# Kernel optimization log

Measured on AMD Instinct MI355X. Metric: run time of the kernel, lower is better.

Reference implementation:

```python
import jax, jax.numpy as jnp
import numpy as np
import math

B, S, D = 2, 2048, 768
H, KS, VS = 12, 64, 64
MAX_DIST, NUM_BASES, MIN_HALF_LIFE = 1000, 16, 3.0


def _exponential_basis_features():
    # positions -max_dist..max_dist, exponential basis as in RelativePositionalBias
    positions = np.arange(-MAX_DIST, MAX_DIST + 1)
    abs_pos = np.abs(positions).astype(np.float32)
    max_range = math.log2(MAX_DIST)
    half_lives = np.power(2.0, np.linspace(MIN_HALF_LIFE, max_range, NUM_BASES)).reshape(1, -1)
    feats = np.exp(-math.log(2.0) * abs_pos[:, None] / half_lives)  # [2*max_dist+1, num_bases]
    return jnp.asarray(feats, dtype=jnp.float32)


def setup_inputs() -> dict:
    key = jax.random.key(0)
    ks = jax.random.split(key, 6)
    x = jax.random.normal(ks[0], (B, S, D), dtype=jnp.float32)
    # torch nn.Linear weight convention: [out_features, in_features], applied as x @ W.T
    Wq = jax.random.normal(ks[1], (H * KS, D), dtype=jnp.float32) * 0.02
    Wk = jax.random.normal(ks[2], (H * KS, D), dtype=jnp.float32) * 0.02
    Wv = jax.random.normal(ks[3], (H * VS, D), dtype=jnp.float32) * 0.02
    # original zero-inits w_o; use small random for a non-degenerate correctness baseline
    Wo = jax.random.normal(ks[4], (D, H * VS), dtype=jnp.float32) * 0.02
    basis_weights = jax.random.normal(ks[5], (H, NUM_BASES), dtype=jnp.float32)
    basis_features = _exponential_basis_features()  # buffer (non-learned)
    return {"x": x, "Wq": Wq, "Wk": Wk, "Wv": Wv, "Wo": Wo,
            "basis_weights": basis_weights, "basis_features": basis_features}


def _relative_bias(basis_features, basis_weights, q_len, k_len):
    rel = jnp.arange(k_len)[None, :] - jnp.arange(q_len)[:, None]
    rel = jnp.clip(rel, -MAX_DIST, MAX_DIST) + MAX_DIST  # [q, k] indices
    basis = basis_features[rel]                          # [q, k, nb]
    return jnp.einsum('qkb,hb->hqk', basis, basis_weights)


def reference(x, Wq, Wk, Wv, Wo, basis_weights, basis_features):
    b, s, _ = x.shape
    q = (x @ Wq.T).reshape(b, s, H, KS)
    k = (x @ Wk.T).reshape(b, s, H, KS)
    v = (x @ Wv.T).reshape(b, s, H, VS)
    scale = math.sqrt(KS)
    scores = jnp.einsum('bqhc,bkhc->bhqk', q, k) / scale
    scores = scores + _relative_bias(basis_features, basis_weights, s, s)[None]
    attn = jax.nn.softmax(scores, axis=-1)  # dropout is identity in eval
    out = jnp.einsum('bhqk,bkhv->bqhv', attn, v).reshape(b, s, H * VS)
    out = out @ Wo.T
    return out, attn
```

## Files before the change

kernel.cpp:

```cpp
#include <hip/hip_runtime.h>

typedef _Float16 f16;
typedef __attribute__((ext_vector_type(8))) _Float16 f16x8;
typedef __attribute__((ext_vector_type(4))) float f32x4;
typedef __attribute__((ext_vector_type(16))) float f32x16;

#define B_ 2
#define S_ 2048
#define DMODEL 768
#define H_ 12
#define HS 64
#define NB_ 16
#define QKV_LD 2304

#define ZERO16 {0.f,0.f,0.f,0.f,0.f,0.f,0.f,0.f,0.f,0.f,0.f,0.f,0.f,0.f,0.f,0.f}

__device__ __forceinline__ void gload16(const f16* g, f16* lds) {
    __builtin_amdgcn_global_load_lds((const __attribute__((address_space(1))) void*)g,
                                     (__attribute__((address_space(3))) void*)lds, 16, 0, 0);
}

__global__ __launch_bounds__(256) void prep_kernel(const float* __restrict__ x,
                                                   const float* __restrict__ Wq,
                                                   const float* __restrict__ Wk,
                                                   const float* __restrict__ Wv,
                                                   const float* __restrict__ Wo,
                                                   const float* __restrict__ bw,
                                                   const float* __restrict__ bf,
                                                   f16* __restrict__ xb,
                                                   f16* __restrict__ wqkv16,
                                                   f16* __restrict__ wo16,
                                                   float* __restrict__ biasTab) {
    int bid = blockIdx.x;
    int t = threadIdx.x;
    if (bid < 5376) {
        const float* src;
        f16* dst;
        float scale = 1.0f;
        int i;
        if (bid < 3072) {
            i = bid * 256 + t; src = x; dst = xb;
        } else if (bid < 4800) {
            i = (bid - 3072) * 256 + t;
            dst = wqkv16;
            if (i < 147456)      { src = Wq; scale = 0.18033688011112f; }
            else if (i < 294912) { src = Wk - 147456 * 4; }
            else                 { src = Wv - 294912 * 4; }
        } else {
            i = (bid - 4800) * 256 + t; src = Wo; dst = wo16;
        }
        float4 v = reinterpret_cast<const float4*>(src)[i];
        union { f16 h[4]; unsigned long long u; } o;
        o.h[0] = (f16)(v.x * scale);
        o.h[1] = (f16)(v.y * scale);
        o.h[2] = (f16)(v.z * scale);
        o.h[3] = (f16)(v.w * scale);
        reinterpret_cast<unsigned long long*>(dst)[i] = o.u;
    } else {
        int idx = (bid - 5376) * 256 + t;
        if (idx >= H_ * 4095) return;
        int h = idx / 4095, d = idx % 4095;
        int rel = min(1000, max(-1000, d - 2047));
        int r = rel + 1000;
        float s = 0.f;
#pragma unroll
        for (int tt = 0; tt < NB_; ++tt) s += bf[r * NB_ + tt] * bw[h * NB_ + tt];
        biasTab[h * 4095 + d] = s * 1.44269504088896f;
    }
}

__global__ __launch_bounds__(256) void vtrans_kernel(const f16* __restrict__ qkv,
                                                     f16* __restrict__ vt) {
    __shared__ f16 tile[64][72];
    int blk = blockIdx.x;
    int tb = blk & 31;
    int bh = blk >> 5;
    int b = bh / H_;
    int tok0 = tb << 6;
    int t = threadIdx.x;
    const f16* src = qkv + (size_t)b * S_ * QKV_LD + 1536 + (bh - b * H_) * 64;
#pragma unroll
    for (int j = 0; j < 2; ++j) {
        int u = t + (j << 8);
        int r = u >> 3, c = (u & 7) << 3;
        *reinterpret_cast<f16x8*>(&tile[r][c]) =
            *reinterpret_cast<const f16x8*>(src + (size_t)(tok0 + r) * QKV_LD + c);
    }
    __syncthreads();
    f16* dst = vt + (size_t)bh * 64 * S_ + tok0;
#pragma unroll
    for (int j = 0; j < 2; ++j) {
        int u = t + (j << 8);
        int v = u >> 3, tc = (u & 7) << 3;
        union { f16 h8[8]; f16x8 v8; } o;
#pragma unroll
        for (int i = 0; i < 8; ++i) o.h8[i] = tile[tc + i][v];
        *reinterpret_cast<f16x8*>(&dst[(size_t)v * S_ + tc]) = o.v8;
    }
}

template <typename OutT>
__global__ __launch_bounds__(256) void gemm_nt(const f16* __restrict__ A,
                                               const f16* __restrict__ Bm,
                                               OutT* __restrict__ C,
                                               int M, int N, int K, float alpha) {
    __shared__ __align__(16) f16 As[128 * 32];
    __shared__ __align__(16) f16 Bs[128 * 32];
    const int tiles_n = N >> 7;
    int tm = blockIdx.x / tiles_n, tn = blockIdx.x % tiles_n;
    int m0 = tm << 7, n0 = tn << 7;
    int t = threadIdx.x;
    int w = t >> 6, l = t & 63;
    int wr = w >> 1, wc = w & 1;
    int fr = l & 15, hi = l >> 4;
    f32x4 acc[4][4] = {};

    for (int k0 = 0; k0 < K; k0 += 32) {
#pragma unroll
        for (int j = 0; j < 2; ++j) {
            int u = t + (j << 8);
            int row = u >> 2, ch = u & 3;
            int gcol = k0 + ((ch ^ (row & 3)) << 3);
            gload16(&A[(size_t)(m0 + row) * K + gcol], As + (w << 9) + (j << 11));
            gload16(&Bm[(size_t)(n0 + row) * K + gcol], Bs + (w << 9) + (j << 11));
        }
        __syncthreads();
        f16x8 af[4], bfv[4];
#pragma unroll
        for (int m = 0; m < 4; ++m) {
            int row = wr * 64 + m * 16 + fr;
            af[m] = *reinterpret_cast<const f16x8*>(&As[row * 32 + ((hi ^ (fr & 3)) << 3)]);
        }
#pragma unroll
        for (int n = 0; n < 4; ++n) {
            int row = wc * 64 + n * 16 + fr;
            bfv[n] = *reinterpret_cast<const f16x8*>(&Bs[row * 32 + ((hi ^ (fr & 3)) << 3)]);
        }
#pragma unroll
        for (int m = 0; m < 4; ++m)
#pragma unroll
            for (int n = 0; n < 4; ++n)
                acc[m][n] = __builtin_amdgcn_mfma_f32_16x16x32_f16(af[m], bfv[n], acc[m][n], 0, 0, 0);
        __syncthreads();
    }
    int cc = l & 15, cr = (l >> 4) << 2;
#pragma unroll
    for (int m = 0; m < 4; ++m)
#pragma unroll
        for (int n = 0; n < 4; ++n)
#pragma unroll
            for (int j = 0; j < 4; ++j) {
                int rg = m0 + wr * 64 + m * 16 + cr + j;
                int cg = n0 + wc * 64 + n * 16 + cc;
                C[(size_t)rg * N + cg] = (OutT)(acc[m][n][j] * alpha);
            }
}

__global__ __launch_bounds__(256, 4) void attn_kernel(const f16* __restrict__ qp,
                                                      const f16* __restrict__ kp,
                                                      const f16* __restrict__ vt,
                                                      const float* __restrict__ biasTab,
                                                      float* __restrict__ attn_out,
                                                      f16* __restrict__ ctx_out) {
    __shared__ __align__(16) union {
        f16 ks1[128 * 64];
        struct { f16 ks[64 * 64]; f16 vs[64 * 64]; } p2;
    } ar;
    __shared__ __align__(16) f16 psh[64][72];
    __shared__ float bias_l[2112];
    __shared__ float red_l[64][2];
    __shared__ float li_s[64];

    int orig = blockIdx.x;
    int blk = (orig & 7) * 96 + (orig >> 3);
    int qt = blk & 31;
    int bh = blk >> 5;
    int h = bh % H_;
    int b = bh / H_;
    int q0 = qt << 6;

    int t = threadIdx.x;
    int w = t >> 6, l = t & 63;
    int wq = w >> 1, wk = w & 1;
    int col = l & 31;
    int hi = l >> 5;
    int hi4 = hi << 2, hi8 = hi << 3;

    const size_t rowbase = (size_t)b * S_ * QKV_LD + (size_t)h * HS;
    const f16* vbase = vt + (size_t)bh * HS * S_;

    f16x8 qf[4];
    {
        const f16* qrow = qp + rowbase + (size_t)(q0 + wq * 32 + col) * QKV_LD + hi8;
#pragma unroll
        for (int ci = 0; ci < 4; ++ci) qf[ci] = *reinterpret_cast<const f16x8*>(qrow + ci * 16);
    }

    {
        const float* bt = biasTab + h * 4095 + (1984 - q0);
        for (int i = t; i < 2111; i += 256) bias_l[i] = bt[i];
    }

    float lsum[16];
#pragma unroll
    for (int r = 0; r < 16; ++r) lsum[r] = 0.f;

    for (int kb0 = 0; kb0 < S_; kb0 += 128) {
#pragma unroll
        for (int j = 0; j < 4; ++j) {
            int u = t + (j << 8);
            int row = u >> 3, ch = u & 7;
            gload16(kp + rowbase + (size_t)(kb0 + row) * QKV_LD + ((ch ^ (row & 7)) << 3),
                    ar.ks1 + (w << 9) + (j << 11));
        }
        __syncthreads();
#pragma unroll
        for (int half = 0; half < 2; ++half) {
            int krow = half * 64 + wk * 32 + col;
            f32x16 s = ZERO16;
#pragma unroll
            for (int ci = 0; ci < 4; ++ci) {
                f16x8 kf = *reinterpret_cast<const f16x8*>(
                    &ar.ks1[krow * 64 + (((ci * 2 + hi) ^ (col & 7)) << 3)]);
                s = __builtin_amdgcn_mfma_f32_32x32x16_f16(qf[ci], kf, s, 0, 0, 0);
            }
            int kcol = kb0 + krow;
            const float* bl = bias_l + (kcol + 63 - (wq * 32 + hi4));
#pragma unroll
            for (int r = 0; r < 16; ++r) {
                const int cr = (r & 3) + 8 * (r >> 2);
                lsum[r] += __builtin_amdgcn_exp2f(s[r] + bl[-cr]);
            }
        }
        __syncthreads();
    }

#pragma unroll
    for (int off = 1; off < 32; off <<= 1) {
#pragma unroll
        for (int r = 0; r < 16; ++r) lsum[r] += __shfl_xor(lsum[r], off);
    }
    if (col == 0) {
#pragma unroll
        for (int r = 0; r < 16; ++r)
            red_l[wq * 32 + (r & 3) + 8 * (r >> 2) + hi4][wk] = lsum[r];
    }
    __syncthreads();
    if (t < 64) li_s[t] = 1.0f / (red_l[t][0] + red_l[t][1]);
    __syncthreads();
    float lreg[16];
#pragma unroll
    for (int r = 0; r < 16; ++r) lreg[r] = li_s[wq * 32 + (r & 3) + 8 * (r >> 2) + hi4];

    f32x16 oacc = ZERO16;
    float* aout = attn_out + (((size_t)b * H_ + h) * S_ + q0) * S_;

    for (int kb0 = 0; kb0 < S_; kb0 += 64) {
#pragma unroll
        for (int j = 0; j < 2; ++j) {
            int u = t + (j << 8);
            int row = u >> 3, ch = u & 7;
            int sw = ((ch ^ (row & 7)) << 3);
            gload16(kp + rowbase + (size_t)(kb0 + row) * QKV_LD + sw,
                    ar.p2.ks + (w << 9) + (j << 11));
            gload16(vbase + (size_t)row * S_ + kb0 + sw,
                    ar.p2.vs + (w << 9) + (j << 11));
        }
        __syncthreads();
        int krow = wk * 32 + col;
        f32x16 s = ZERO16;
#pragma unroll
        for (int ci = 0; ci < 4; ++ci) {
            f16x8 kf = *reinterpret_cast<const f16x8*>(
                &ar.p2.ks[krow * 64 + (((ci * 2 + hi) ^ (col & 7)) << 3)]);
            s = __builtin_amdgcn_mfma_f32_32x32x16_f16(qf[ci], kf, s, 0, 0, 0);
        }
        int kcol = kb0 + krow;
        const float* bl = bias_l + (kcol + 63 - (wq * 32 + hi4));
#pragma unroll
        for (int r = 0; r < 16; ++r) {
            const int cr = (r & 3) + 8 * (r >> 2);
            int row = wq * 32 + cr + hi4;
            float p = __builtin_amdgcn_exp2f(s[r] + bl[-cr]) * lreg[r];
            __builtin_nontemporal_store(p, &aout[(size_t)row * S_ + kcol]);
            psh[row][wk * 32 + col] = (f16)p;
        }
        __syncthreads();
#pragma unroll
        for (int ci = 0; ci < 4; ++ci) {
            f16x8 pa = *reinterpret_cast<const f16x8*>(&psh[wq * 32 + col][ci * 16 + hi8]);
            f16x8 vf = *reinterpret_cast<const f16x8*>(
                &ar.p2.vs[krow * 64 + (((ci * 2 + hi) ^ (col & 7)) << 3)]);
            oacc = __builtin_amdgcn_mfma_f32_32x32x16_f16(pa, vf, oacc, 0, 0, 0);
        }
        __syncthreads();
    }

    {
        f16* cbase = ctx_out + ((size_t)b * S_ + q0) * DMODEL + h * HS + wk * 32 + col;
#pragma unroll
        for (int r = 0; r < 16; ++r) {
            int row = wq * 32 + (r & 3) + 8 * (r >> 2) + hi4;
            cbase[(size_t)row * DMODEL] = (f16)oacc[r];
        }
    }
}

extern "C" void kernel_launch(void* const* d_in, const int* in_sizes, int n_in,
                              void* d_out, int out_size, void* d_ws, size_t ws_size,
                              hipStream_t stream) {
    const float* x     = (const float*)d_in[0];
    const float* Wq    = (const float*)d_in[1];
    const float* Wk    = (const float*)d_in[2];
    const float* Wv    = (const float*)d_in[3];
    const float* Wo    = (const float*)d_in[4];
    const float* bw    = (const float*)d_in[5];
    const float* bfeat = (const float*)d_in[6];

    char* ws = (char*)d_ws;
    f16*   xb      = (f16*)(ws + 0);
    f16*   vt      = (f16*)(ws + 0);
    f16*   qkv     = (f16*)(ws + 6291456);
    f16*   ctx     = (f16*)(ws + 25165824);
    f16*   wqkv16  = (f16*)(ws + 31457280);
    f16*   wo16    = (f16*)(ws + 34996224);
    float* biasTab = (float*)(ws + 36175872);

    float* out0 = (float*)d_out;
    float* attn = out0 + (size_t)B_ * S_ * DMODEL;

    prep_kernel<<<5568, 256, 0, stream>>>(x, Wq, Wk, Wv, Wo, bw, bfeat,
                                          xb, wqkv16, wo16, biasTab);

    gemm_nt<f16><<<32 * 18, 256, 0, stream>>>(xb, wqkv16, qkv, 4096, QKV_LD, 768, 1.0f);

    vtrans_kernel<<<768, 256, 0, stream>>>(qkv, vt);

    attn_kernel<<<B_ * H_ * (S_ / 64), 256, 0, stream>>>(
        qkv + 0, qkv + 768, vt, biasTab, attn, ctx);

    gemm_nt<float><<<32 * 6, 256, 0, stream>>>(ctx, wo16, out0, 4096, DMODEL, 768, 1.0f);
}
```

Baseline: 177.7 us.

## Transpose QK MFMA so P stays in registers and attn stores vectorize

Swaps the MFMA operand order so each lane owns one query row and holds contiguous key columns. This lets the softmax row sum be a single per-lane scalar with one shuffle, turns the attention-probability stores into 16-byte vector stores, and feeds P to the PV MFMA through register shuffles instead of a shared-memory staging buffer. Each wave now computes partial outputs over all 64 value columns for its half of the keys, and the two halves are combined through shared memory at the end. The costs are extra accumulator registers and a final cross-wave reduction.

```diff
diff --git a/kernel.cpp b/kernel.cpp
--- a/kernel.cpp
+++ b/kernel.cpp
@@ -1,6 +1,8 @@
 #include <hip/hip_runtime.h>
 
 typedef _Float16 f16;
+typedef __attribute__((ext_vector_type(2))) __fp16 h16x2;
+typedef __attribute__((ext_vector_type(4))) _Float16 f16x4;
 typedef __attribute__((ext_vector_type(8))) _Float16 f16x8;
 typedef __attribute__((ext_vector_type(4))) float f32x4;
 typedef __attribute__((ext_vector_type(16))) float f32x16;
@@ -49,7 +51,7 @@
         } else {
             i = (bid - 4800) * 256 + t; src = Wo; dst = wo16;
         }
-        float4 v = reinterpret_cast<const float4*>(src)[i];
+        f32x4 v = reinterpret_cast<const f32x4*>(src)[i];
         union { f16 h[4]; unsigned long long u; } o;
         o.h[0] = (f16)(v.x * scale);
         o.h[1] = (f16)(v.y * scale);
@@ -165,11 +167,10 @@
     __shared__ __align__(16) union {
         f16 ks1[128 * 64];
         struct { f16 ks[64 * 64]; f16 vs[64 * 64]; } p2;
+        float red[4096];
     } ar;
-    __shared__ __align__(16) f16 psh[64][72];
     __shared__ float bias_l[2112];
     __shared__ float red_l[64][2];
-    __shared__ float li_s[64];
 
     int orig = blockIdx.x;
     int blk = (orig & 7) * 96 + (orig >> 3);
@@ -182,16 +183,16 @@
     int t = threadIdx.x;
     int w = t >> 6, l = t & 63;
     int wq = w >> 1, wk = w & 1;
-    int col = l & 31;
+    int ql = l & 31;
     int hi = l >> 5;
-    int hi4 = hi << 2, hi8 = hi << 3;
+    int hi8 = hi << 3;
 
     const size_t rowbase = (size_t)b * S_ * QKV_LD + (size_t)h * HS;
     const f16* vbase = vt + (size_t)bh * HS * S_;
 
     f16x8 qf[4];
     {
-        const f16* qrow = qp + rowbase + (size_t)(q0 + wq * 32 + col) * QKV_LD + hi8;
+        const f16* qrow = qp + rowbase + (size_t)(q0 + wq * 32 + ql) * QKV_LD + hi8;
 #pragma unroll
         for (int ci = 0; ci < 4; ++ci) qf[ci] = *reinterpret_cast<const f16x8*>(qrow + ci * 16);
     }
@@ -201,10 +202,7 @@
         for (int i = t; i < 2111; i += 256) bias_l[i] = bt[i];
     }
 
-    float lsum[16];
-#pragma unroll
-    for (int r = 0; r < 16; ++r) lsum[r] = 0.f;
-
+    float lsum = 0.f;
     for (int kb0 = 0; kb0 < S_; kb0 += 128) {
 #pragma unroll
         for (int j = 0; j < 4; ++j) {
@@ -214,46 +212,32 @@
                     ar.ks1 + (w << 9) + (j << 11));
         }
         __syncthreads();
+        const float* bl = bias_l + (kb0 + wk * 32 + 63 + (hi << 2) - wq * 32 - ql);
 #pragma unroll
         for (int half = 0; half < 2; ++half) {
-            int krow = half * 64 + wk * 32 + col;
+            int arow = half * 64 + wk * 32 + ql;
             f32x16 s = ZERO16;
 #pragma unroll
             for (int ci = 0; ci < 4; ++ci) {
                 f16x8 kf = *reinterpret_cast<const f16x8*>(
-                    &ar.ks1[krow * 64 + (((ci * 2 + hi) ^ (col & 7)) << 3)]);
-                s = __builtin_amdgcn_mfma_f32_32x32x16_f16(qf[ci], kf, s, 0, 0, 0);
+                    &ar.ks1[arow * 64 + (((ci * 2 + hi) ^ (arow & 7)) << 3)]);
+                s = __builtin_amdgcn_mfma_f32_32x32x16_f16(kf, qf[ci], s, 0, 0, 0);
             }
-            int kcol = kb0 + krow;
-            const float* bl = bias_l + (kcol + 63 - (wq * 32 + hi4));
-#pragma unroll
-            for (int r = 0; r < 16; ++r) {
-                const int cr = (r & 3) + 8 * (r >> 2);
-                lsum[r] += __builtin_amdgcn_exp2f(s[r] + bl[-cr]);
-            }
-        }
-        __syncthreads();
-    }
-
-#pragma unroll
-    for (int off = 1; off < 32; off <<= 1) {
-#pragma unroll
-        for (int r = 0; r < 16; ++r) lsum[r] += __shfl_xor(lsum[r], off);
-    }
-    if (col == 0) {
-#pragma unroll
-        for (int r = 0; r < 16; ++r)
-            red_l[wq * 32 + (r & 3) + 8 * (r >> 2) + hi4][wk] = lsum[r];
-    }
+            const float* blh = bl + half * 64;
+#pragma unroll
+            for (int r = 0; r < 16; ++r)
+                lsum += __builtin_amdgcn_exp2f(s[r] + blh[((r >> 2) << 3) + (r & 3)]);
+        }
+        __syncthreads();
+    }
+    lsum += __shfl_xor(lsum, 32);
+    if (hi == 0) red_l[wq * 32 + ql][wk] = lsum;
     __syncthreads();
-    if (t < 64) li_s[t] = 1.0f / (red_l[t][0] + red_l[t][1]);
-    __syncthreads();
-    float lreg[16];
-#pragma unroll
-    for (int r = 0; r < 16; ++r) lreg[r] = li_s[wq * 32 + (r & 3) + 8 * (r >> 2) + hi4];
-
-    f32x16 oacc = ZERO16;
-    float* aout = attn_out + (((size_t)b * H_ + h) * S_ + q0) * S_;
+    const float lreg = 1.0f / (red_l[wq * 32 + ql][0] + red_l[wq * 32 + ql][1]);
+
+    f32x16 oacc0 = ZERO16, oacc1 = ZERO16;
+    float* arow_out = attn_out + (((size_t)b * H_ + h) * S_ + q0) * S_
+                    + (size_t)(wq * 32 + ql) * S_;
 
     for (int kb0 = 0; kb0 < S_; kb0 += 64) {
 #pragma unroll
@@ -267,41 +251,81 @@
                     ar.p2.vs + (w << 9) + (j << 11));
         }
         __syncthreads();
-        int krow = wk * 32 + col;
+        int arow = wk * 32 + ql;
         f32x16 s = ZERO16;
 #pragma unroll
         for (int ci = 0; ci < 4; ++ci) {
             f16x8 kf = *reinterpret_cast<const f16x8*>(
-                &ar.p2.ks[krow * 64 + (((ci * 2 + hi) ^ (col & 7)) << 3)]);
-            s = __builtin_amdgcn_mfma_f32_32x32x16_f16(qf[ci], kf, s, 0, 0, 0);
-        }
-        int kcol = kb0 + krow;
-        const float* bl = bias_l + (kcol + 63 - (wq * 32 + hi4));
+                &ar.p2.ks[arow * 64 + (((ci * 2 + hi) ^ (arow & 7)) << 3)]);
+            s = __builtin_amdgcn_mfma_f32_32x32x16_f16(kf, qf[ci], s, 0, 0, 0);
+        }
+        const float* bl = bias_l + (kb0 + wk * 32 + 63 + (hi << 2) - wq * 32 - ql);
+        unsigned w2[8];
+#pragma unroll
+        for (int r4 = 0; r4 < 4; ++r4) {
+            float p0 = __builtin_amdgcn_exp2f(s[4 * r4 + 0] + bl[8 * r4 + 0]) * lreg;
+            float p1 = __builtin_amdgcn_exp2f(s[4 * r4 + 1] + bl[8 * r4 + 1]) * lreg;
+            float p2 = __builtin_amdgcn_exp2f(s[4 * r4 + 2] + bl[8 * r4 + 2]) * lreg;
+            float p3 = __builtin_amdgcn_exp2f(s[4 * r4 + 3] + bl[8 * r4 + 3]) * lreg;
+            f32x4 st = {p0, p1, p2, p3};
+            __builtin_nontemporal_store(st, reinterpret_cast<f32x4*>(
+                arow_out + kb0 + wk * 32 + 8 * r4 + (hi << 2)));
+            union { h16x2 h; unsigned u; } c0, c1;
+            c0.h = __builtin_amdgcn_cvt_pkrtz(p0, p1);
+            c1.h = __builtin_amdgcn_cvt_pkrtz(p2, p3);
+            w2[2 * r4] = c0.u;
+            w2[2 * r4 + 1] = c1.u;
+        }
+        unsigned sw2[8];
+#pragma unroll
+        for (int i = 0; i < 8; ++i) sw2[i] = __shfl_xor(w2[i], 32);
+#pragma unroll
+        for (int vh = 0; vh < 2; ++vh) {
+            int vrow = vh * 32 + ql;
+#pragma unroll
+            for (int ci = 0; ci < 2; ++ci) {
+                f16x8 vf = *reinterpret_cast<const f16x8*>(
+                    &ar.p2.vs[vrow * 64 + (((wk * 4 + ci * 2 + hi) ^ (vrow & 7)) << 3)]);
+                int bb = ci * 4 + (hi << 1);
+                union { unsigned u[4]; f16x8 v; } pf;
+                pf.u[0] = hi ? sw2[bb] : w2[bb];
+                pf.u[1] = hi ? sw2[bb + 1] : w2[bb + 1];
+                pf.u[2] = hi ? w2[bb] : sw2[bb];
+                pf.u[3] = hi ? w2[bb + 1] : sw2[bb + 1];
+                if (vh == 0)
+                    oacc0 = __builtin_amdgcn_mfma_f32_32x32x16_f16(vf, pf.v, oacc0, 0, 0, 0);
+                else
+                    oacc1 = __builtin_amdgcn_mfma_f32_32x32x16_f16(vf, pf.v, oacc1, 0, 0, 0);
+            }
+        }
+        __syncthreads();
+    }
+
+    if (wk == 1) {
 #pragma unroll
         for (int r = 0; r < 16; ++r) {
-            const int cr = (r & 3) + 8 * (r >> 2);
-            int row = wq * 32 + cr + hi4;
-            float p = __builtin_amdgcn_exp2f(s[r] + bl[-cr]) * lreg[r];
-            __builtin_nontemporal_store(p, &aout[(size_t)row * S_ + kcol]);
-            psh[row][wk * 32 + col] = (f16)p;
-        }
-        __syncthreads();
-#pragma unroll
-        for (int ci = 0; ci < 4; ++ci) {
-            f16x8 pa = *reinterpret_cast<const f16x8*>(&psh[wq * 32 + col][ci * 16 + hi8]);
-            f16x8 vf = *reinterpret_cast<const f16x8*>(
-                &ar.p2.vs[krow * 64 + (((ci * 2 + hi) ^ (col & 7)) << 3)]);
-            oacc = __builtin_amdgcn_mfma_f32_32x32x16_f16(pa, vf, oacc, 0, 0, 0);
-        }
-        __syncthreads();
-    }
-
-    {
-        f16* cbase = ctx_out + ((size_t)b * S_ + q0) * DMODEL + h * HS + wk * 32 + col;
-#pragma unroll
-        for (int r = 0; r < 16; ++r) {
-            int row = wq * 32 + (r & 3) + 8 * (r >> 2) + hi4;
-            cbase[(size_t)row * DMODEL] = (f16)oacc[r];
+            int v = (r & 3) + ((r >> 2) << 3) + (hi << 2);
+            ar.red[wq * 2048 + v * 32 + ql] = oacc0[r];
+            ar.red[wq * 2048 + (v + 32) * 32 + ql] = oacc1[r];
+        }
+    }
+    __syncthreads();
+    if (wk == 0) {
+        f16* cbase = ctx_out + ((size_t)b * S_ + q0 + wq * 32 + ql) * DMODEL + h * HS;
+#pragma unroll
+        for (int vh = 0; vh < 2; ++vh) {
+#pragma unroll
+            for (int r4 = 0; r4 < 4; ++r4) {
+                f16x4 o4;
+#pragma unroll
+                for (int rr = 0; rr < 4; ++rr) {
+                    int r = 4 * r4 + rr;
+                    int v = vh * 32 + rr + (r4 << 3) + (hi << 2);
+                    float own = (vh == 0) ? oacc0[r] : oacc1[r];
+                    o4[rr] = (f16)(own + ar.red[wq * 2048 + v * 32 + ql]);
+                }
+                *reinterpret_cast<f16x4*>(cbase + vh * 32 + (r4 << 3) + (hi << 2)) = o4;
+            }
         }
     }
 }
```

Result: slower. 327.7 us (+84.4%).

## Load K/V fragments directly into registers with prefetch, double-buffer P tile

Applied to the files above, without the earlier changes.

The attention kernel no longer stages K and V tiles through shared memory. Each wave loads its MFMA operand fragments straight from global memory into registers and prefetches the next tile while the current one computes. The P tile is double-buffered in a swizzled shared buffer, so each iteration needs one barrier instead of several. The price is more register pressure (launch bounds lowered from 4 to 3 blocks per SM) and uncoalesced, redundant global reads of K/V across waves.

```diff
diff --git a/kernel.cpp b/kernel.cpp
--- a/kernel.cpp
+++ b/kernel.cpp
@@ -1,6 +1,7 @@
 #include <hip/hip_runtime.h>
 
 typedef _Float16 f16;
+typedef __attribute__((ext_vector_type(4))) _Float16 f16x4;
 typedef __attribute__((ext_vector_type(8))) _Float16 f16x8;
 typedef __attribute__((ext_vector_type(4))) float f32x4;
 typedef __attribute__((ext_vector_type(16))) float f32x16;
@@ -49,7 +50,7 @@
         } else {
             i = (bid - 4800) * 256 + t; src = Wo; dst = wo16;
         }
-        float4 v = reinterpret_cast<const float4*>(src)[i];
+        f32x4 v = reinterpret_cast<const f32x4*>(src)[i];
         union { f16 h[4]; unsigned long long u; } o;
         o.h[0] = (f16)(v.x * scale);
         o.h[1] = (f16)(v.y * scale);
@@ -156,17 +157,14 @@
             }
 }
 
-__global__ __launch_bounds__(256, 4) void attn_kernel(const f16* __restrict__ qp,
+#define PSWZ(row) ((((row) >> 2) & 3) << 3)
+__global__ __launch_bounds__(256, 3) void attn_kernel(const f16* __restrict__ qp,
                                                       const f16* __restrict__ kp,
                                                       const f16* __restrict__ vt,
                                                       const float* __restrict__ biasTab,
                                                       float* __restrict__ attn_out,
                                                       f16* __restrict__ ctx_out) {
-    __shared__ __align__(16) union {
-        f16 ks1[128 * 64];
-        struct { f16 ks[64 * 64]; f16 vs[64 * 64]; } p2;
-    } ar;
-    __shared__ __align__(16) f16 psh[64][72];
+    __shared__ __align__(16) f16 psh[2][64][72];
     __shared__ float bias_l[2112];
     __shared__ float red_l[64][2];
     __shared__ float li_s[64];
@@ -182,7 +180,7 @@
     int t = threadIdx.x;
     int w = t >> 6, l = t & 63;
     int wq = w >> 1, wk = w & 1;
-    int col = l & 31;
+    int ql = l & 31;
     int hi = l >> 5;
     int hi4 = hi << 2, hi8 = hi << 3;
 
@@ -191,7 +189,7 @@
 
     f16x8 qf[4];
     {
-        const f16* qrow = qp + rowbase + (size_t)(q0 + wq * 32 + col) * QKV_LD + hi8;
+        const f16* qrow = qp + rowbase + (size_t)(q0 + wq * 32 + ql) * QKV_LD + hi8;
 #pragma unroll
         for (int ci = 0; ci < 4; ++ci) qf[ci] = *reinterpret_cast<const f16x8*>(qrow + ci * 16);
     }
@@ -200,39 +198,41 @@
         const float* bt = biasTab + h * 4095 + (1984 - q0);
         for (int i = t; i < 2111; i += 256) bias_l[i] = bt[i];
     }
+    __syncthreads();
 
     float lsum[16];
 #pragma unroll
     for (int r = 0; r < 16; ++r) lsum[r] = 0.f;
 
-    for (int kb0 = 0; kb0 < S_; kb0 += 128) {
-#pragma unroll
-        for (int j = 0; j < 4; ++j) {
-            int u = t + (j << 8);
-            int row = u >> 3, ch = u & 7;
-            gload16(kp + rowbase + (size_t)(kb0 + row) * QKV_LD + ((ch ^ (row & 7)) << 3),
-                    ar.ks1 + (w << 9) + (j << 11));
-        }
-        __syncthreads();
-#pragma unroll
-        for (int half = 0; half < 2; ++half) {
-            int krow = half * 64 + wk * 32 + col;
-            f32x16 s = ZERO16;
-#pragma unroll
-            for (int ci = 0; ci < 4; ++ci) {
-                f16x8 kf = *reinterpret_cast<const f16x8*>(
-                    &ar.ks1[krow * 64 + (((ci * 2 + hi) ^ (col & 7)) << 3)]);
-                s = __builtin_amdgcn_mfma_f32_32x32x16_f16(qf[ci], kf, s, 0, 0, 0);
-            }
-            int kcol = kb0 + krow;
-            const float* bl = bias_l + (kcol + 63 - (wq * 32 + hi4));
-#pragma unroll
-            for (int r = 0; r < 16; ++r) {
-                const int cr = (r & 3) + 8 * (r >> 2);
-                lsum[r] += __builtin_amdgcn_exp2f(s[r] + bl[-cr]);
-            }
-        }
-        __syncthreads();
+    f16x8 kc0, kc1, kc2, kc3;
+    {
+        const f16* kr = kp + rowbase + (size_t)(wk * 32 + ql) * QKV_LD + hi8;
+        kc0 = *reinterpret_cast<const f16x8*>(kr);
+        kc1 = *reinterpret_cast<const f16x8*>(kr + 16);
+        kc2 = *reinterpret_cast<const f16x8*>(kr + 32);
+        kc3 = *reinterpret_cast<const f16x8*>(kr + 48);
+    }
+    for (int j = 0; j < 32; ++j) {
+        int kt = j * 64 + wk * 32;
+        f32x16 s = ZERO16;
+        s = __builtin_amdgcn_mfma_f32_32x32x16_f16(qf[0], kc0, s, 0, 0, 0);
+        s = __builtin_amdgcn_mfma_f32_32x32x16_f16(qf[1], kc1, s, 0, 0, 0);
+        s = __builtin_amdgcn_mfma_f32_32x32x16_f16(qf[2], kc2, s, 0, 0, 0);
+        s = __builtin_amdgcn_mfma_f32_32x32x16_f16(qf[3], kc3, s, 0, 0, 0);
+        {
+            int nkt = (j < 31) ? kt + 64 : wk * 32;
+            const f16* kr = kp + rowbase + (size_t)(nkt + ql) * QKV_LD + hi8;
+            kc0 = *reinterpret_cast<const f16x8*>(kr);
+            kc1 = *reinterpret_cast<const f16x8*>(kr + 16);
+            kc2 = *reinterpret_cast<const f16x8*>(kr + 32);
+            kc3 = *reinterpret_cast<const f16x8*>(kr + 48);
+        }
+        const float* bl = bias_l + (kt + ql + 63 - wq * 32 - hi4);
+#pragma unroll
+        for (int r = 0; r < 16; ++r) {
+            const int cr = (r & 3) + 8 * (r >> 2);
+            lsum[r] += __builtin_amdgcn_exp2f(s[r] + bl[-cr]);
+        }
     }
 
 #pragma unroll
@@ -240,7 +240,7 @@
 #pragma unroll
         for (int r = 0; r < 16; ++r) lsum[r] += __shfl_xor(lsum[r], off);
     }
-    if (col == 0) {
+    if (ql == 0) {
 #pragma unroll
         for (int r = 0; r < 16; ++r)
             red_l[wq * 32 + (r & 3) + 8 * (r >> 2) + hi4][wk] = lsum[r];
@@ -254,50 +254,73 @@
 
     f32x16 oacc = ZERO16;
     float* aout = attn_out + (((size_t)b * H_ + h) * S_ + q0) * S_;
-
-    for (int kb0 = 0; kb0 < S_; kb0 += 64) {
-#pragma unroll
-        for (int j = 0; j < 2; ++j) {
-            int u = t + (j << 8);
-            int row = u >> 3, ch = u & 7;
-            int sw = ((ch ^ (row & 7)) << 3);
-            gload16(kp + rowbase + (size_t)(kb0 + row) * QKV_LD + sw,
-                    ar.p2.ks + (w << 9) + (j << 11));
-            gload16(vbase + (size_t)row * S_ + kb0 + sw,
-                    ar.p2.vs + (w << 9) + (j << 11));
-        }
-        __syncthreads();
-        int krow = wk * 32 + col;
+    const int kcol_loc = wk * 32 + ql;
+
+    f16x8 vc0, vc1, vc2, vc3;
+    {
+        const f16* kr = kp + rowbase + (size_t)kcol_loc * QKV_LD + hi8;
+        kc0 = *reinterpret_cast<const f16x8*>(kr);
+        kc1 = *reinterpret_cast<const f16x8*>(kr + 16);
+        kc2 = *reinterpret_cast<const f16x8*>(kr + 32);
+        kc3 = *reinterpret_cast<const f16x8*>(kr + 48);
+        const f16* vr = vbase + (size_t)kcol_loc * S_ + hi8;
+        vc0 = *reinterpret_cast<const f16x8*>(vr);
+        vc1 = *reinterpret_cast<const f16x8*>(vr + 16);
+        vc2 = *reinterpret_cast<const f16x8*>(vr + 32);
+        vc3 = *reinterpret_cast<const f16x8*>(vr + 48);
+    }
+
+    for (int tix = 0; tix < 32; ++tix) {
+        int kb0 = tix << 6;
+        int kcol = kb0 + kcol_loc;
+        int nkb = (tix < 31) ? kb0 + 64 : 0;
         f32x16 s = ZERO16;
-#pragma unroll
-        for (int ci = 0; ci < 4; ++ci) {
-            f16x8 kf = *reinterpret_cast<const f16x8*>(
-                &ar.p2.ks[krow * 64 + (((ci * 2 + hi) ^ (col & 7)) << 3)]);
-            s = __builtin_amdgcn_mfma_f32_32x32x16_f16(qf[ci], kf, s, 0, 0, 0);
-        }
-        int kcol = kb0 + krow;
-        const float* bl = bias_l + (kcol + 63 - (wq * 32 + hi4));
+        s = __builtin_amdgcn_mfma_f32_32x32x16_f16(qf[0], kc0, s, 0, 0, 0);
+        s = __builtin_amdgcn_mfma_f32_32x32x16_f16(qf[1], kc1, s, 0, 0, 0);
+        s = __builtin_amdgcn_mfma_f32_32x32x16_f16(qf[2], kc2, s, 0, 0, 0);
+        s = __builtin_amdgcn_mfma_f32_32x32x16_f16(qf[3], kc3, s, 0, 0, 0);
+        {
+            const f16* kr = kp + rowbase + (size_t)(nkb + kcol_loc) * QKV_LD + hi8;
+            kc0 = *reinterpret_cast<const f16x8*>(kr);
+            kc1 = *reinterpret_cast<const f16x8*>(kr + 16);
+            kc2 = *reinterpret_cast<const f16x8*>(kr + 32);
+            kc3 = *reinterpret_cast<const f16x8*>(kr + 48);
+        }
+        const int buf = tix & 1;
+        const float* bl = bias_l + (kcol + 63 - wq * 32 - hi4);
 #pragma unroll
         for (int r = 0; r < 16; ++r) {
             const int cr = (r & 3) + 8 * (r >> 2);
             int row = wq * 32 + cr + hi4;
             float p = __builtin_amdgcn_exp2f(s[r] + bl[-cr]) * lreg[r];
             __builtin_nontemporal_store(p, &aout[(size_t)row * S_ + kcol]);
-            psh[row][wk * 32 + col] = (f16)p;
-        }
-        __syncthreads();
-#pragma unroll
-        for (int ci = 0; ci < 4; ++ci) {
-            f16x8 pa = *reinterpret_cast<const f16x8*>(&psh[wq * 32 + col][ci * 16 + hi8]);
-            f16x8 vf = *reinterpret_cast<const f16x8*>(
-                &ar.p2.vs[krow * 64 + (((ci * 2 + hi) ^ (col & 7)) << 3)]);
-            oacc = __builtin_amdgcn_mfma_f32_32x32x16_f16(pa, vf, oacc, 0, 0, 0);
-        }
-        __syncthreads();
-    }
-
-    {
-        f16* cbase = ctx_out + ((size_t)b * S_ + q0) * DMODEL + h * HS + wk * 32 + col;
+            psh[buf][row][kcol_loc ^ PSWZ(row)] = (f16)p;
+        }
+        asm volatile("s_waitcnt lgkmcnt(0)" ::: "memory");
+        __builtin_amdgcn_s_barrier();
+        {
+            const int rowq = wq * 32 + ql;
+            const int sw = PSWZ(rowq);
+            f16x8 pa0 = *reinterpret_cast<const f16x8*>(&psh[buf][rowq][(0  + hi8) ^ sw]);
+            f16x8 pa1 = *reinterpret_cast<const f16x8*>(&psh[buf][rowq][(16 + hi8) ^ sw]);
+            f16x8 pa2 = *reinterpret_cast<const f16x8*>(&psh[buf][rowq][(32 + hi8) ^ sw]);
+            f16x8 pa3 = *reinterpret_cast<const f16x8*>(&psh[buf][rowq][(48 + hi8) ^ sw]);
+            oacc = __builtin_amdgcn_mfma_f32_32x32x16_f16(pa0, vc0, oacc, 0, 0, 0);
+            oacc = __builtin_amdgcn_mfma_f32_32x32x16_f16(pa1, vc1, oacc, 0, 0, 0);
+            oacc = __builtin_amdgcn_mfma_f32_32x32x16_f16(pa2, vc2, oacc, 0, 0, 0);
+            oacc = __builtin_amdgcn_mfma_f32_32x32x16_f16(pa3, vc3, oacc, 0, 0, 0);
+        }
+        {
+            const f16* vr = vbase + (size_t)kcol_loc * S_ + nkb + hi8;
+            vc0 = *reinterpret_cast<const f16x8*>(vr);
+            vc1 = *reinterpret_cast<const f16x8*>(vr + 16);
+            vc2 = *reinterpret_cast<const f16x8*>(vr + 32);
+            vc3 = *reinterpret_cast<const f16x8*>(vr + 48);
+        }
+    }
+
+    {
+        f16* cbase = ctx_out + ((size_t)b * S_ + q0) * DMODEL + h * HS + kcol_loc;
 #pragma unroll
         for (int r = 0; r < 16; ++r) {
             int row = wq * 32 + (r & 3) + 8 * (r >> 2) + hi4;
```

Measured after the change: 214.7 us. +20.8%, slower.

## Double-buffer LDS tiles in GEMM and attention loops with async prefetch

Applied to the files above, without the earlier changes.

Adds two LDS buffers for the GEMM tiles and for the K/V tiles in both attention passes. The next tile is prefetched with global_load_lds while the current one is computed, and each iteration ends with an explicit vmcnt wait plus barrier. The P staging buffer gains an XOR swizzle to reduce LDS bank conflicts, and the P-to-PV barrier now waits only on LDS counters. The larger LDS footprint lowers the attention occupancy hint from 4 to 3 blocks per CU, which may cost latency hiding.

```diff
diff --git a/kernel.cpp b/kernel.cpp
--- a/kernel.cpp
+++ b/kernel.cpp
@@ -1,6 +1,7 @@
 #include <hip/hip_runtime.h>
 
 typedef _Float16 f16;
+typedef __attribute__((ext_vector_type(4))) _Float16 f16x4;
 typedef __attribute__((ext_vector_type(8))) _Float16 f16x8;
 typedef __attribute__((ext_vector_type(4))) float f32x4;
 typedef __attribute__((ext_vector_type(16))) float f32x16;
@@ -19,6 +20,8 @@
     __builtin_amdgcn_global_load_lds((const __attribute__((address_space(1))) void*)g,
                                      (__attribute__((address_space(3))) void*)lds, 16, 0, 0);
 }
+#define WAIT_VM0_BARRIER()  do { asm volatile("s_waitcnt vmcnt(0)" ::: "memory"); \
+                                 __builtin_amdgcn_s_barrier(); } while (0)
 
 __global__ __launch_bounds__(256) void prep_kernel(const float* __restrict__ x,
                                                    const float* __restrict__ Wq,
@@ -49,7 +52,7 @@
         } else {
             i = (bid - 4800) * 256 + t; src = Wo; dst = wo16;
         }
-        float4 v = reinterpret_cast<const float4*>(src)[i];
+        f32x4 v = reinterpret_cast<const f32x4*>(src)[i];
         union { f16 h[4]; unsigned long long u; } o;
         o.h[0] = (f16)(v.x * scale);
         o.h[1] = (f16)(v.y * scale);
@@ -104,8 +107,8 @@
                                                const f16* __restrict__ Bm,
                                                OutT* __restrict__ C,
                                                int M, int N, int K, float alpha) {
-    __shared__ __align__(16) f16 As[128 * 32];
-    __shared__ __align__(16) f16 Bs[128 * 32];
+    __shared__ __align__(16) f16 As[2][128 * 32];
+    __shared__ __align__(16) f16 Bs[2][128 * 32];
     const int tiles_n = N >> 7;
     int tm = blockIdx.x / tiles_n, tn = blockIdx.x % tiles_n;
     int m0 = tm << 7, n0 = tn << 7;
@@ -115,34 +118,43 @@
     int fr = l & 15, hi = l >> 4;
     f32x4 acc[4][4] = {};
 
-    for (int k0 = 0; k0 < K; k0 += 32) {
-#pragma unroll
-        for (int j = 0; j < 2; ++j) {
-            int u = t + (j << 8);
-            int row = u >> 2, ch = u & 3;
-            int gcol = k0 + ((ch ^ (row & 3)) << 3);
-            gload16(&A[(size_t)(m0 + row) * K + gcol], As + (w << 9) + (j << 11));
-            gload16(&Bm[(size_t)(n0 + row) * K + gcol], Bs + (w << 9) + (j << 11));
-        }
-        __syncthreads();
+#define GEMM_STAGE(buf, k0)                                                        \
+    do {                                                                           \
+        _Pragma("unroll")                                                          \
+        for (int j = 0; j < 2; ++j) {                                              \
+            int u = t + (j << 8);                                                  \
+            int row = u >> 2, ch = u & 3;                                          \
+            int gcol = (k0) + ((ch ^ (row & 3)) << 3);                             \
+            gload16(&A[(size_t)(m0 + row) * K + gcol], As[buf] + (w << 9) + (j << 11)); \
+            gload16(&Bm[(size_t)(n0 + row) * K + gcol], Bs[buf] + (w << 9) + (j << 11)); \
+        }                                                                          \
+    } while (0)
+
+    const int nk = K >> 5;
+    GEMM_STAGE(0, 0);
+    WAIT_VM0_BARRIER();
+    for (int kt = 0; kt < nk; ++kt) {
+        int buf = kt & 1;
+        if (kt + 1 < nk) GEMM_STAGE(buf ^ 1, (kt + 1) << 5);
         f16x8 af[4], bfv[4];
 #pragma unroll
         for (int m = 0; m < 4; ++m) {
             int row = wr * 64 + m * 16 + fr;
-            af[m] = *reinterpret_cast<const f16x8*>(&As[row * 32 + ((hi ^ (fr & 3)) << 3)]);
+            af[m] = *reinterpret_cast<const f16x8*>(&As[buf][row * 32 + ((hi ^ (fr & 3)) << 3)]);
         }
 #pragma unroll
         for (int n = 0; n < 4; ++n) {
             int row = wc * 64 + n * 16 + fr;
-            bfv[n] = *reinterpret_cast<const f16x8*>(&Bs[row * 32 + ((hi ^ (fr & 3)) << 3)]);
+            bfv[n] = *reinterpret_cast<const f16x8*>(&Bs[buf][row * 32 + ((hi ^ (fr & 3)) << 3)]);
         }
 #pragma unroll
         for (int m = 0; m < 4; ++m)
 #pragma unroll
             for (int n = 0; n < 4; ++n)
                 acc[m][n] = __builtin_amdgcn_mfma_f32_16x16x32_f16(af[m], bfv[n], acc[m][n], 0, 0, 0);
-        __syncthreads();
-    }
+        WAIT_VM0_BARRIER();
+    }
+#undef GEMM_STAGE
     int cc = l & 15, cr = (l >> 4) << 2;
 #pragma unroll
     for (int m = 0; m < 4; ++m)
@@ -156,15 +168,16 @@
             }
 }
 
-__global__ __launch_bounds__(256, 4) void attn_kernel(const f16* __restrict__ qp,
+#define PSWZ(row) ((((row) >> 2) & 3) << 3)
+__global__ __launch_bounds__(256, 3) void attn_kernel(const f16* __restrict__ qp,
                                                       const f16* __restrict__ kp,
                                                       const f16* __restrict__ vt,
                                                       const float* __restrict__ biasTab,
                                                       float* __restrict__ attn_out,
                                                       f16* __restrict__ ctx_out) {
     __shared__ __align__(16) union {
-        f16 ks1[128 * 64];
-        struct { f16 ks[64 * 64]; f16 vs[64 * 64]; } p2;
+        f16 ks1[2][128 * 64];
+        struct { f16 ks[2][64 * 64]; f16 vs[2][64 * 64]; } p2;
     } ar;
     __shared__ __align__(16) f16 psh[64][72];
     __shared__ float bias_l[2112];
@@ -201,19 +214,26 @@
         for (int i = t; i < 2111; i += 256) bias_l[i] = bt[i];
     }
 
+#define P1_STAGE(buf, kb0)                                                          \
+    do {                                                                            \
+        _Pragma("unroll")                                                           \
+        for (int j = 0; j < 4; ++j) {                                               \
+            int u = t + (j << 8);                                                   \
+            int row = u >> 3, ch = u & 7;                                           \
+            gload16(kp + rowbase + (size_t)((kb0) + row) * QKV_LD + ((ch ^ (row & 7)) << 3), \
+                    ar.ks1[buf] + (w << 9) + (j << 11));                            \
+        }                                                                           \
+    } while (0)
+
     float lsum[16];
 #pragma unroll
     for (int r = 0; r < 16; ++r) lsum[r] = 0.f;
 
-    for (int kb0 = 0; kb0 < S_; kb0 += 128) {
-#pragma unroll
-        for (int j = 0; j < 4; ++j) {
-            int u = t + (j << 8);
-            int row = u >> 3, ch = u & 7;
-            gload16(kp + rowbase + (size_t)(kb0 + row) * QKV_LD + ((ch ^ (row & 7)) << 3),
-                    ar.ks1 + (w << 9) + (j << 11));
-        }
-        __syncthreads();
+    P1_STAGE(0, 0);
+    WAIT_VM0_BARRIER();
+    for (int jt = 0; jt < 16; ++jt) {
+        int buf = jt & 1;
+        if (jt + 1 < 16) P1_STAGE(buf ^ 1, (jt + 1) << 7);
 #pragma unroll
         for (int half = 0; half < 2; ++half) {
             int krow = half * 64 + wk * 32 + col;
@@ -221,10 +241,10 @@
 #pragma unroll
             for (int ci = 0; ci < 4; ++ci) {
                 f16x8 kf = *reinterpret_cast<const f16x8*>(
-                    &ar.ks1[krow * 64 + (((ci * 2 + hi) ^ (col & 7)) << 3)]);
+                    &ar.ks1[buf][krow * 64 + (((ci * 2 + hi) ^ (krow & 7)) << 3)]);
                 s = __builtin_amdgcn_mfma_f32_32x32x16_f16(qf[ci], kf, s, 0, 0, 0);
             }
-            int kcol = kb0 + krow;
+            int kcol = (jt << 7) + krow;
             const float* bl = bias_l + (kcol + 63 - (wq * 32 + hi4));
 #pragma unroll
             for (int r = 0; r < 16; ++r) {
@@ -232,8 +252,9 @@
                 lsum[r] += __builtin_amdgcn_exp2f(s[r] + bl[-cr]);
             }
         }
-        __syncthreads();
-    }
+        WAIT_VM0_BARRIER();
+    }
+#undef P1_STAGE
 
 #pragma unroll
     for (int off = 1; off < 32; off <<= 1) {
@@ -252,30 +273,38 @@
 #pragma unroll
     for (int r = 0; r < 16; ++r) lreg[r] = li_s[wq * 32 + (r & 3) + 8 * (r >> 2) + hi4];
 
+#define P2_STAGE(buf, kb0)                                                          \
+    do {                                                                            \
+        _Pragma("unroll")                                                           \
+        for (int j = 0; j < 2; ++j) {                                               \
+            int u = t + (j << 8);                                                   \
+            int row = u >> 3, ch = u & 7;                                           \
+            int sw = ((ch ^ (row & 7)) << 3);                                       \
+            gload16(kp + rowbase + (size_t)((kb0) + row) * QKV_LD + sw,             \
+                    ar.p2.ks[buf] + (w << 9) + (j << 11));                          \
+            gload16(vbase + (size_t)row * S_ + (kb0) + sw,                          \
+                    ar.p2.vs[buf] + (w << 9) + (j << 11));                          \
+        }                                                                           \
+    } while (0)
+
     f32x16 oacc = ZERO16;
     float* aout = attn_out + (((size_t)b * H_ + h) * S_ + q0) * S_;
-
-    for (int kb0 = 0; kb0 < S_; kb0 += 64) {
-#pragma unroll
-        for (int j = 0; j < 2; ++j) {
-            int u = t + (j << 8);
-            int row = u >> 3, ch = u & 7;
-            int sw = ((ch ^ (row & 7)) << 3);
-            gload16(kp + rowbase + (size_t)(kb0 + row) * QKV_LD + sw,
-                    ar.p2.ks + (w << 9) + (j << 11));
-            gload16(vbase + (size_t)row * S_ + kb0 + sw,
-                    ar.p2.vs + (w << 9) + (j << 11));
-        }
-        __syncthreads();
-        int krow = wk * 32 + col;
+    const int kcol_loc = wk * 32 + col;
+
+    P2_STAGE(0, 0);
+    WAIT_VM0_BARRIER();
+    for (int tix = 0; tix < 32; ++tix) {
+        int buf = tix & 1;
+        int kb0 = tix << 6;
+        if (tix + 1 < 32) P2_STAGE(buf ^ 1, kb0 + 64);
         f32x16 s = ZERO16;
 #pragma unroll
         for (int ci = 0; ci < 4; ++ci) {
             f16x8 kf = *reinterpret_cast<const f16x8*>(
-                &ar.p2.ks[krow * 64 + (((ci * 2 + hi) ^ (col & 7)) << 3)]);
+                &ar.p2.ks[buf][kcol_loc * 64 + (((ci * 2 + hi) ^ (kcol_loc & 7)) << 3)]);
             s = __builtin_amdgcn_mfma_f32_32x32x16_f16(qf[ci], kf, s, 0, 0, 0);
         }
-        int kcol = kb0 + krow;
+        int kcol = kb0 + kcol_loc;
         const float* bl = bias_l + (kcol + 63 - (wq * 32 + hi4));
 #pragma unroll
         for (int r = 0; r < 16; ++r) {
@@ -283,21 +312,28 @@
             int row = wq * 32 + cr + hi4;
             float p = __builtin_amdgcn_exp2f(s[r] + bl[-cr]) * lreg[r];
             __builtin_nontemporal_store(p, &aout[(size_t)row * S_ + kcol]);
-            psh[row][wk * 32 + col] = (f16)p;
+            psh[row][kcol_loc ^ PSWZ(row)] = (f16)p;
+        }
+        asm volatile("s_waitcnt lgkmcnt(0)" ::: "memory");
+        __builtin_amdgcn_s_barrier();
+        __builtin_amdgcn_sched_barrier(0);
+        {
+            const int rowq = wq * 32 + col;
+            const int sw = PSWZ(rowq);
+#pragma unroll
+            for (int ci = 0; ci < 4; ++ci) {
+                f16x8 pa = *reinterpret_cast<const f16x8*>(&psh[rowq][(ci * 16 + hi8) ^ sw]);
+                f16x8 vf = *reinterpret_cast<const f16x8*>(
+                    &ar.p2.vs[buf][kcol_loc * 64 + (((ci * 2 + hi) ^ (kcol_loc & 7)) << 3)]);
+                oacc = __builtin_amdgcn_mfma_f32_32x32x16_f16(pa, vf, oacc, 0, 0, 0);
+            }
         }
         __syncthreads();
-#pragma unroll
-        for (int ci = 0; ci < 4; ++ci) {
-            f16x8 pa = *reinterpret_cast<const f16x8*>(&psh[wq * 32 + col][ci * 16 + hi8]);
-            f16x8 vf = *reinterpret_cast<const f16x8*>(
-                &ar.p2.vs[krow * 64 + (((ci * 2 + hi) ^ (col & 7)) << 3)]);
-            oacc = __builtin_amdgcn_mfma_f32_32x32x16_f16(pa, vf, oacc, 0, 0, 0);
-        }
-        __syncthreads();
-    }
+    }
+#undef P2_STAGE
 
     {
-        f16* cbase = ctx_out + ((size_t)b * S_ + q0) * DMODEL + h * HS + wk * 32 + col;
+        f16* cbase = ctx_out + ((size_t)b * S_ + q0) * DMODEL + h * HS + kcol_loc;
 #pragma unroll
         for (int r = 0; r < 16; ++r) {
             int row = wq * 32 + (r & 3) + 8 * (r >> 2) + hi4;
```

New measurement: 173.8 us. 1.02x faster.
